# Performance work log

Hardware: AMD Instinct MI355X
Metric: run time of the kernel (lower is better)

The kernel has to match this reference:

```python
import jax, jax.numpy as jnp
import numpy as np

N, E, ESM, H, OUT, L, NG = 20000, 640000, 1280, 128, 256, 3, 64
NV, EV = 4, 1  # node/edge vector channels
MSG_S, MSG_V = 2 * H + H, 2 * NV + EV   # 384, 9
UPD_S, UPD_V = 2 * H, 2 * NV            # 256, 8


def _safe_norm(v):
    # exact ||v|| with zero (not nan) gradient at v == 0
    n2 = jnp.sum(v * v, axis=-1)
    pos = n2 > 0
    return jnp.sqrt(jnp.where(pos, n2, 1.0)) * pos


def _normalize(x, eps=1e-12):
    n = _safe_norm(x)[..., None]
    return jnp.where(n > 0, x / jnp.maximum(n, eps), 0.0)


def _ln(x, g, b, eps=1e-5):
    m = x.mean(-1, keepdims=True)
    v = ((x - m) ** 2).mean(-1, keepdims=True)
    return (x - m) / jnp.sqrt(v + eps) * g + b


def _gvp(s, v, Wss, Wvs, Wsv, Wvv, g, b):
    # s: [M, Cs], v: [M, Cv, 3]
    vn = _safe_norm(v)                                        # [M, Cv]
    s_out = jax.nn.gelu(_ln(s @ Wss.T + vn @ Wvs.T, g, b), approximate=False)
    v_out = jnp.einsum('mic,oi->moc', v, Wvv)                 # [M, Cvo, 3]
    v_out = v_out * jax.nn.sigmoid(s @ Wsv.T)[:, :, None]     # gate from input s
    return s_out, v_out


def _compute_node_vectors(coords, cb):
    ca_cb = _normalize(cb - coords)
    ca_next = jnp.roll(coords, -1, axis=0)
    d = (ca_next - coords).at[-1].set(0.0)
    d = _normalize(d)
    normal = _normalize(jnp.cross(ca_cb, d))
    t = (ca_next - jnp.roll(coords, 1, axis=0)).at[0].set(0.0).at[-1].set(0.0)
    t = _normalize(t)
    return jnp.stack([ca_cb, d, normal, t], axis=1)           # [N, 4, 3]


def setup_inputs() -> dict:
    key = jax.random.key(0)
    ks = jax.random.split(key, 32)

    def w(k, shape):
        return (jax.random.normal(k, shape, jnp.float32) / np.sqrt(shape[-1])).astype(jnp.float32)

    inp = {
        'esm_features': jax.random.normal(ks[0], (N, ESM), jnp.float32),
        'geometric_features': jax.random.normal(ks[1], (N, 15), jnp.float32),
        'node_coords': jax.random.normal(ks[2], (N, 3), jnp.float32) * 10.0,
        'edge_index': jax.random.randint(ks[3], (2, E), 0, N, jnp.int32),
        'edge_attr': jax.random.normal(ks[4], (E, 16), jnp.float32),
        'batch_index': jnp.sort(jax.random.randint(ks[5], (N,), 0, NG, jnp.int32)),
        # projections
        'node_proj_W': w(ks[6], (H, ESM + 9)), 'node_proj_b': jnp.zeros((H,), jnp.float32),
        'edge_proj_W': w(ks[7], (H, 13)), 'edge_proj_b': jnp.zeros((H,), jnp.float32),
        # message GVP (stacked over L layers)
        'msg_Wss': w(ks[8], (L, H, MSG_S)), 'msg_Wvs': w(ks[9], (L, H, MSG_V)),
        'msg_Wsv': w(ks[10], (L, NV, MSG_S)), 'msg_Wvv': w(ks[11], (L, NV, MSG_V)),
        'msg_ln_g': jnp.ones((L, H), jnp.float32), 'msg_ln_b': jnp.zeros((L, H), jnp.float32),
        # update GVP
        'upd_Wss': w(ks[12], (L, H, UPD_S)), 'upd_Wvs': w(ks[13], (L, H, UPD_V)),
        'upd_Wsv': w(ks[14], (L, NV, UPD_S)), 'upd_Wvv': w(ks[15], (L, NV, UPD_V)),
        'upd_ln_g': jnp.ones((L, H), jnp.float32), 'upd_ln_b': jnp.zeros((L, H), jnp.float32),
        # heads
        'node_out_W': w(ks[16], (ESM, H)), 'node_out_b': jnp.zeros((ESM,), jnp.float32),
        'graph_out_W': w(ks[17], (OUT, H)), 'graph_out_b': jnp.zeros((OUT,), jnp.float32),
    }
    return inp


def reference(esm_features, geometric_features, node_coords, edge_index, edge_attr,
              batch_index, node_proj_W, node_proj_b, edge_proj_W, edge_proj_b,
              msg_Wss, msg_Wvs, msg_Wsv, msg_Wvv, msg_ln_g, msg_ln_b,
              upd_Wss, upd_Wvs, upd_Wsv, upd_Wvv, upd_ln_g, upd_ln_b,
              node_out_W, node_out_b, graph_out_W, graph_out_b):
    n = esm_features.shape[0]
    cb = geometric_features[:, 3:6]
    geo_scalar = geometric_features[:, 6:15]
    node_s = jnp.concatenate([esm_features, geo_scalar], -1) @ node_proj_W.T + node_proj_b
    node_v = _compute_node_vectors(node_coords, cb)
    edge_s = jnp.concatenate([edge_attr[:, 0:2], edge_attr[:, 5:]], -1) @ edge_proj_W.T + edge_proj_b
    edge_v = edge_attr[:, 2:5][:, None, :]                    # [E, 1, 3]
    src, dst = edge_index[0], edge_index[1]
    for l in range(msg_Wss.shape[0]):
        ms = jnp.concatenate([node_s[src], node_s[dst], edge_s], -1)   # [E, 3H]
        mv = jnp.concatenate([node_v[src], node_v[dst], edge_v], 1)    # [E, 9, 3]
        ms, mv = _gvp(ms, mv, msg_Wss[l], msg_Wvs[l], msg_Wsv[l], msg_Wvv[l],
                      msg_ln_g[l], msg_ln_b[l])
        ag_s = jnp.zeros((n, ms.shape[1]), ms.dtype).at[dst].add(ms)
        ag_v = jnp.zeros((n, mv.shape[1], 3), mv.dtype).at[dst].add(mv)
        us = jnp.concatenate([node_s, ag_s], -1)
        uv = jnp.concatenate([node_v, ag_v], 1)
        ns, nv = _gvp(us, uv, upd_Wss[l], upd_Wvs[l], upd_Wsv[l], upd_Wvv[l],
                      upd_ln_g[l], upd_ln_b[l])
        node_s = node_s + ns
        node_v = node_v + nv
    updated_nodes = node_s @ node_out_W.T + node_out_b
    gfeat = node_s @ graph_out_W.T + graph_out_b
    cnt = jax.ops.segment_sum(jnp.ones((n,), gfeat.dtype), batch_index, NG)
    graph_emb = jax.ops.segment_sum(gfeat, batch_index, NG) / jnp.maximum(cnt, 1.0)[:, None]
    return graph_emb, updated_nodes
```

## Files before the change

kernel.cpp:

```cpp
#include <hip/hip_runtime.h>
#include <math.h>

#define DEVI __device__ __forceinline__

namespace {

constexpr int NN = 20000;
constexpr int NE = 640000;

DEVI float gelu_f(float x){ return 0.5f*x*(1.0f+erff(x*0.70710678118654752440f)); }
DEVI float gelu_t(float x){
  float u = x*x;
  float z = x*(1.59576912f + 0.07135481f*u);
  return x / (1.f + __expf(-z));
}
DEVI float sigm(float x){ return 1.0f/(1.0f+expf(-x)); }
DEVI float sigm_f(float x){ return 1.0f/(1.0f+__expf(-x)); }

struct F3{ float x,y,z; };
DEVI F3 sub3(F3 a, F3 b){ return F3{a.x-b.x, a.y-b.y, a.z-b.z}; }
DEVI F3 cross3(F3 a, F3 b){ return F3{a.y*b.z-a.z*b.y, a.z*b.x-a.x*b.z, a.x*b.y-a.y*b.x}; }
DEVI F3 snorm3(F3 v){
  float n2 = v.x*v.x+v.y*v.y+v.z*v.z;
  if(n2 > 0.f){ float inv = 1.0f/sqrtf(n2); return F3{v.x*inv, v.y*inv, v.z*inv}; }
  return F3{0.f,0.f,0.f};
}

__global__ void k_prep(const float* __restrict__ npW, const float* __restrict__ noW,
                       const float* __restrict__ goW,
                       const float* __restrict__ mWss, const float* __restrict__ mWvs,
                       const float* __restrict__ uWss, const float* __restrict__ uWvs,
                       float* __restrict__ Wt_np, float* __restrict__ Wt_no,
                       float* __restrict__ Wt_go,
                       float* __restrict__ Wt_mss, float* __restrict__ Wt_mvs,
                       float* __restrict__ Wt_uss, float* __restrict__ Wt_uvs){
  int b = blockIdx.x, t = threadIdx.x;
  const float* src; float* dst; int R,C,ld,base,elems;
  if(b<645){ src=npW; dst=Wt_np; R=128;C=1289;ld=1289; base=0; elems=164992; }
  else if(b<1285){ src=noW; dst=Wt_no; R=1280;C=128;ld=128; base=645; elems=163840; }
  else if(b<1413){ src=goW; dst=Wt_go; R=256;C=128;ld=128; base=1285; elems=32768; }
  else {
    int bb=b-1413; int l=bb/265; int r=bb-l*265;
    if(r<128){ src=mWss+(size_t)l*128*384; dst=Wt_mss+(size_t)l*256*128; R=128;C=256;ld=384; base=1413+l*265; elems=32768; }
    else if(r<133){ src=mWvs+(size_t)l*128*9; dst=Wt_mvs+(size_t)l*9*128; R=128;C=9;ld=9; base=1413+l*265+128; elems=1152; }
    else if(r<261){ src=uWss+(size_t)l*128*256; dst=Wt_uss+(size_t)l*256*128; R=128;C=256;ld=256; base=1413+l*265+133; elems=32768; }
    else { src=uWvs+(size_t)l*128*8; dst=Wt_uvs+(size_t)l*8*128; R=128;C=8;ld=8; base=1413+l*265+261; elems=1024; }
  }
  int idx=(b-base)*256+t;
  if(idx>=elems) return;
  int r=idx/C, c=idx%C;
  dst[c*R+r] = src[r*ld+c];
}

__global__ __launch_bounds__(256,4) void k_init(
                       const float* __restrict__ esm, const float* __restrict__ geo,
                       const float* __restrict__ Wt, const float* __restrict__ bias,
                       float* __restrict__ node_s){
  __shared__ float s_l[16][64];
  int t = threadIdx.x;
  int o = t&127, h = t>>7;
  int n0 = blockIdx.x*16;
  float acc[8];
#pragma unroll
  for(int i=0;i<8;i++) acc[i]=0.f;
  for(int k0=0;k0<1289;k0+=64){
    int kmax = (1289-k0 < 64) ? (1289-k0) : 64;
    for(int idx=t; idx<1024; idx+=256){
      int n = idx>>6, k = idx&63;
      float v = 0.f;
      int kk = k0+k;
      if(k < kmax){
        v = (kk<1280) ? esm[(size_t)(n0+n)*1280 + kk] : geo[(n0+n)*15 + 6 + (kk-1280)];
      }
      s_l[n][k] = v;
    }
    __syncthreads();
    int kq = kmax & ~3;
    for(int k=0;k<kq;k+=4){
      float w0 = Wt[(k0+k)*128+o];
      float w1 = Wt[(k0+k+1)*128+o];
      float w2 = Wt[(k0+k+2)*128+o];
      float w3 = Wt[(k0+k+3)*128+o];
#pragma unroll
      for(int n=0;n<8;n++){
        float4 s4 = *reinterpret_cast<const float4*>(&s_l[h*8+n][k]);
        acc[n] += s4.x*w0 + s4.y*w1 + s4.z*w2 + s4.w*w3;
      }
    }
    for(int k=kq;k<kmax;k++){
      float w = Wt[(k0+k)*128+o];
#pragma unroll
      for(int n=0;n<8;n++) acc[n] += s_l[h*8+n][k]*w;
    }
    __syncthreads();
  }
  float b = bias[o];
#pragma unroll
  for(int n=0;n<8;n++) node_s[(size_t)(n0+h*8+n)*128 + o] = acc[n] + b;
}

__global__ void k_nodevec(const float* __restrict__ coords, const float* __restrict__ geo,
                          float* __restrict__ node_v,
                          int* __restrict__ counts, int* __restrict__ cntg){
  int n = blockIdx.x*256 + threadIdx.x;
  if(n<64) cntg[n]=0;
  if(n>=NN) return;
  counts[n]=0;
  F3 c  {coords[n*3], coords[n*3+1], coords[n*3+2]};
  F3 cb {geo[n*15+3], geo[n*15+4], geo[n*15+5]};
  F3 cacb = snorm3(sub3(cb, c));
  F3 d{0.f,0.f,0.f};
  if(n < NN-1){
    F3 nx {coords[(n+1)*3], coords[(n+1)*3+1], coords[(n+1)*3+2]};
    d = snorm3(sub3(nx, c));
  }
  F3 nor = snorm3(cross3(cacb, d));
  F3 tv{0.f,0.f,0.f};
  if(n>0 && n<NN-1){
    F3 nx {coords[(n+1)*3], coords[(n+1)*3+1], coords[(n+1)*3+2]};
    F3 pv {coords[(n-1)*3], coords[(n-1)*3+1], coords[(n-1)*3+2]};
    tv = snorm3(sub3(nx, pv));
  }
  float* p = node_v + n*12;
  p[0]=cacb.x; p[1]=cacb.y; p[2]=cacb.z;
  p[3]=d.x;    p[4]=d.y;    p[5]=d.z;
  p[6]=nor.x;  p[7]=nor.y;  p[8]=nor.z;
  p[9]=tv.x;   p[10]=tv.y;  p[11]=tv.z;
}

__global__ void k_hist(const int* __restrict__ eidx, const int* __restrict__ batch,
                       int* __restrict__ counts, int* __restrict__ cntg){
  int i = blockIdx.x*256+threadIdx.x;
  if(i<NE) atomicAdd(&counts[eidx[NE+i]], 1);
  if(i<NN) atomicAdd(&cntg[batch[i]], 1);
}
__global__ void k_scan1(const int* __restrict__ counts, int* __restrict__ bsums){
  __shared__ int red[256];
  int b=blockIdx.x, t=threadIdx.x;
  int base=b*512;
  int v=0;
  for(int i=t;i<512;i+=256){ int g=base+i; if(g<NN) v+=counts[g]; }
  red[t]=v; __syncthreads();
  for(int s=128;s;s>>=1){ if(t<s) red[t]+=red[t+s]; __syncthreads(); }
  if(t==0) bsums[b]=red[0];
}
__global__ void k_scan23(const int* __restrict__ counts, const int* __restrict__ bsums,
                         int* __restrict__ offs, int* __restrict__ cursor){
  __shared__ int c_l[512];
  int b=blockIdx.x, t=threadIdx.x, base=b*512;
  for(int i=t;i<512;i+=256){ int g=base+i; c_l[i] = (g<NN)? counts[g]:0; }
  __syncthreads();
  if(t==0){
    int run=0;
    for(int i=0;i<b;i++) run += bsums[i];
    for(int i=0;i<512;i++){
      int g=base+i;
      if(g<NN){ offs[g]=run; cursor[g]=run; }
      run += c_l[i];
    }
    if(b==39) offs[NN]=run;
  }
}
__global__ void k_fill(const int* __restrict__ eidx, int* __restrict__ cursor,
                       const float* __restrict__ eattr,
                       int* __restrict__ srcp, float* __restrict__ ea_s){
  int e = blockIdx.x*256+threadIdx.x;
  if(e>=NE) return;
  int d = eidx[NE+e];
  int s = eidx[e];
  int pos = atomicAdd(&cursor[d], 1);
  srcp[pos] = s;
  const float4* src4 = reinterpret_cast<const float4*>(eattr + (size_t)e*16);
  float4* dst4 = reinterpret_cast<float4*>(ea_s + (size_t)pos*16);
  dst4[0]=src4[0]; dst4[1]=src4[1]; dst4[2]=src4[2]; dst4[3]=src4[3];
}

__global__ __launch_bounds__(256,4) void k_pre(
                      const float* __restrict__ node_s, const float* __restrict__ node_v,
                      const float* __restrict__ Wt_ss, const float* __restrict__ Wt_vs,
                      const float* __restrict__ Wsv, const float* __restrict__ Wvv,
                      float* __restrict__ P_a, float* __restrict__ P_b,
                      float* __restrict__ G_a, float* __restrict__ G_b,
                      float* __restrict__ V_a, float* __restrict__ V_b){
  __shared__ float s_l[16][128];
  __shared__ float nv_l[16][4];
  __shared__ float uv[16][12];
  int t = threadIdx.x;
  int n0 = blockIdx.x*16;
  for(int idx=t; idx<2048; idx+=256){
    int n = idx>>7, k = idx&127;
    s_l[n][k] = node_s[(size_t)(n0+n)*128 + k];
  }
  if(t<192){ int n=t/12, k=t%12; uv[n][k] = node_v[(n0+n)*12+k]; }
  __syncthreads();
  if(t<64){
    int n=t>>2, j=t&3;
    float x=uv[n][j*3], y=uv[n][j*3+1], z=uv[n][j*3+2];
    float n2=x*x+y*y+z*z;
    nv_l[n][j] = n2>0.f ? sqrtf(n2) : 0.f;
  }
  if(t<192){
    int n=t/12, k=t%12, c=k/3, x=k-c*3;
    float va=0.f, vb=0.f;
#pragma unroll
    for(int j=0;j<4;j++){
      float vv = uv[n][j*3+x];
      va += Wvv[c*9+j]*vv;
      vb += Wvv[c*9+4+j]*vv;
    }
    V_a[(n0+n)*12+k]=va; V_b[(n0+n)*12+k]=vb;
  }
  if(t<128){
    int n=t>>3, c=(t>>1)&3, hh=t&1;
    const float* w = Wsv + c*384 + hh*128;
    float g=0.f;
    for(int k=0;k<128;k++) g += s_l[n][k]*w[k];
    (hh ? G_b : G_a)[(n0+n)*4+c] = g;
  }
  __syncthreads();
  int o = t&127, h = t>>7;
  float acc[16];
#pragma unroll
  for(int i=0;i<16;i++) acc[i]=0.f;
  const float* Wb = Wt_ss + h*128*128;
  for(int k=0;k<128;k++){
    float w = Wb[k*128+o];
#pragma unroll
    for(int n=0;n<16;n++) acc[n] += s_l[n][k]*w;
  }
  const float* Wv = Wt_vs + h*4*128;
#pragma unroll
  for(int j=0;j<4;j++){
    float w = Wv[j*128+o];
#pragma unroll
    for(int n=0;n<16;n++) acc[n] += nv_l[n][j]*w;
  }
  float* P = h ? P_b : P_a;
#pragma unroll
  for(int n=0;n<16;n++) P[(size_t)(n0+n)*128+o] = acc[n];
}

__global__ void k_econst3(const float* __restrict__ mWss, const float* __restrict__ mWvs,
                          const float* __restrict__ mWsv, const float* __restrict__ mWvv,
                          const float* __restrict__ Wep, const float* __restrict__ epb,
                          float* __restrict__ econ){
  int l = blockIdx.x;
  const float* Wss = mWss + (size_t)l*128*384;
  const float* Wvs = mWvs + (size_t)l*128*9;
  const float* Wsv = mWsv + (size_t)l*4*384;
  const float* Wvv = mWvv + (size_t)l*4*9;
  float* ec = econ + (size_t)l*2048;
  int t=threadIdx.x;
  for(int idx=t; idx<13*128; idx+=256){
    int j=idx>>7, o=idx&127;
    float s=0.f;
    for(int k=0;k<128;k++) s += Wss[o*384+256+k]*Wep[k*13+j];
    ec[j*128+o]=s;
  }
  for(int o=t;o<128;o+=256){
    float s=0.f;
    for(int k=0;k<128;k++) s += Wss[o*384+256+k]*epb[k];
    ec[1664+o]=s;
    ec[1792+o]=Wvs[o*9+8];
  }
  if(t<52){ int c=t/13,j=t%13; float s=0.f; for(int k=0;k<128;k++) s+=Wsv[c*384+256+k]*Wep[k*13+j]; ec[1920+t]=s; }
  if(t<4){ float s=0.f; for(int k=0;k<128;k++) s+=Wsv[t*384+256+k]*epb[k]; ec[1972+t]=s; ec[1976+t]=Wvv[t*9+8]; }
}

#define DECLST(P) int P##s=0; float4 P##A0{},P##A1{},P##A2{},P##A3{}; \
                  float P##pax=0.f,P##pay=0.f,P##ga=0.f,P##va=0.f;
#define LOADST(P, IDX) do{ int _p=(IDX); \
  P##s = srcp[_p]; \
  const float4* _ea = reinterpret_cast<const float4*>(ea_s + (size_t)_p*16); \
  P##A0=_ea[0]; P##A1=_ea[1]; P##A2=_ea[2]; P##A3=_ea[3]; \
  const float* _pa = P_a + (size_t)P##s*128; \
  P##pax=_pa[lane]; P##pay=_pa[64+lane]; \
  if(lane<12){ P##ga=G_a[(size_t)P##s*4+cv]; P##va=V_a[(size_t)P##s*12+lane]; } \
}while(0)
#define COMPUTE(P) do{ \
  float e0=P##A0.x,e1=P##A0.y,e2=P##A1.y,e3=P##A1.z,e4=P##A1.w, \
        e5=P##A2.x,e6=P##A2.y,e7=P##A2.z,e8=P##A2.w,e9=P##A3.x, \
        e10=P##A3.y,e11=P##A3.z,e12=P##A3.w; \
  float evx=P##A0.z, evy=P##A0.w, evz=P##A1.x; \
  float en2 = evx*evx+evy*evy+evz*evz; \
  float evn = en2>0.f ? sqrtf(en2) : 0.f; \
  float px = fmaf(evn,W8x, P##pax + Bx); \
  float py = fmaf(evn,W8y, P##pay + By); \
  px=fmaf(me2x[0],e0,px);   py=fmaf(me2y[0],e0,py); \
  px=fmaf(me2x[1],e1,px);   py=fmaf(me2y[1],e1,py); \
  px=fmaf(me2x[2],e2,px);   py=fmaf(me2y[2],e2,py); \
  px=fmaf(me2x[3],e3,px);   py=fmaf(me2y[3],e3,py); \
  px=fmaf(me2x[4],e4,px);   py=fmaf(me2y[4],e4,py); \
  px=fmaf(me2x[5],e5,px);   py=fmaf(me2y[5],e5,py); \
  px=fmaf(me2x[6],e6,px);   py=fmaf(me2y[6],e6,py); \
  px=fmaf(me2x[7],e7,px);   py=fmaf(me2y[7],e7,py); \
  px=fmaf(me2x[8],e8,px);   py=fmaf(me2y[8],e8,py); \
  px=fmaf(me2x[9],e9,px);   py=fmaf(me2y[9],e9,py); \
  px=fmaf(me2x[10],e10,px); py=fmaf(me2y[10],e10,py); \
  px=fmaf(me2x[11],e11,px); py=fmaf(me2y[11],e11,py); \
  px=fmaf(me2x[12],e12,px); py=fmaf(me2y[12],e12,py); \
  float sm = px+py; \
  float sq = px*px + py*py; \
  _Pragma("unroll") \
  for(int m=32;m;m>>=1){ sm += __shfl_xor(sm,m); sq += __shfl_xor(sq,m); } \
  float mean = sm*0.0078125f; \
  float var  = fmaf(sq,0.0078125f, -mean*mean); \
  float rstd = rsqrtf((var>0.f?var:0.f) + 1e-5f); \
  accx += gelu_t(fmaf((px-mean)*rstd, LGx, LBx)); \
  accy += gelu_t(fmaf((py-mean)*rstd, LGy, LBy)); \
  if(lane<12){ \
    float g = P##ga + gbc; \
    g=fmaf(grc[0],e0,g); g=fmaf(grc[1],e1,g); g=fmaf(grc[2],e2,g); \
    g=fmaf(grc[3],e3,g); g=fmaf(grc[4],e4,g); g=fmaf(grc[5],e5,g); \
    g=fmaf(grc[6],e6,g); g=fmaf(grc[7],e7,g); g=fmaf(grc[8],e8,g); \
    g=fmaf(grc[9],e9,g); g=fmaf(grc[10],e10,g); g=fmaf(grc[11],e11,g); \
    g=fmaf(grc[12],e12,g); \
    float gt = sigm_f(g); \
    float evc = (xv==0) ? evx : ((xv==1) ? evy : evz); \
    avk = fmaf(fmaf(wvc,evc, P##va + vbk), gt, avk); \
  } \
}while(0)

__global__ __launch_bounds__(256,2) void k_msg(
                      const float* __restrict__ P_a, const float* __restrict__ P_b,
                      const float* __restrict__ G_a, const float* __restrict__ G_b,
                      const float* __restrict__ V_a, const float* __restrict__ V_b,
                      const float* __restrict__ ea_s, const int* __restrict__ srcp,
                      const int* __restrict__ offs,
                      const float* __restrict__ ec,
                      const float* __restrict__ lng, const float* __restrict__ lnb,
                      float* __restrict__ ag_s, float* __restrict__ ag_v){
  int t = threadIdx.x;
  int n = blockIdx.x*4 + (t>>6);
  int lane = t&63;
  float me2x[13], me2y[13];
#pragma unroll
  for(int j=0;j<13;j++){ me2x[j]=ec[j*128+lane]; me2y[j]=ec[j*128+64+lane]; }
  float Bx = ec[1664+lane]    + P_b[(size_t)n*128+lane];
  float By = ec[1664+64+lane] + P_b[(size_t)n*128+64+lane];
  float W8x = ec[1792+lane], W8y = ec[1792+64+lane];
  float LGx = lng[lane], LGy = lng[64+lane];
  float LBx = lnb[lane], LBy = lnb[64+lane];
  int cv = lane/3, xv = lane - cv*3;
  int cvg = (lane<12) ? cv : 0;
  float grc[13];
#pragma unroll
  for(int j=0;j<13;j++) grc[j] = ec[1920 + cvg*13 + j];
  float vbk=0.f, gbc=0.f, wvc=0.f;
  if(lane<12){
    vbk = V_b[(size_t)n*12+lane];
    gbc = G_b[(size_t)n*4+cv] + ec[1972+cv];
    wvc = ec[1976+cv];
  }
  float accx=0.f, accy=0.f, avk=0.f;
  int beg = offs[n], end = offs[n+1];
  DECLST(a_) DECLST(b_)
  int idx = beg;
  if(beg < end) LOADST(a_, beg);
  while(idx + 1 < end){
    LOADST(b_, idx+1);
    COMPUTE(a_);
    if(idx + 2 < end) LOADST(a_, idx+2);
    COMPUTE(b_);
    idx += 2;
  }
  if(idx < end) COMPUTE(a_);
  ag_s[(size_t)n*128+lane]    = accx;
  ag_s[(size_t)n*128+64+lane] = accy;
  if(lane<12) ag_v[(size_t)n*12+lane] = avk;
}

__global__ __launch_bounds__(256,4) void k_update(
                         float* __restrict__ node_s, float* __restrict__ node_v,
                         const float* __restrict__ ag_s, const float* __restrict__ ag_v,
                         const float* __restrict__ Wt_ss, const float* __restrict__ Wt_vs,
                         const float* __restrict__ Wsv, const float* __restrict__ Wvv,
                         const float* __restrict__ lng, const float* __restrict__ lnb){
  __shared__ float us[16][257];
  __shared__ float pre[16][129];
  __shared__ float uv[16][24];
  __shared__ float uvn[16][8];
  __shared__ float stats[16][2];
  __shared__ float gate_l[16][4];
  int t = threadIdx.x;
  int n0 = blockIdx.x*16;
  for(int idx=t; idx<2048; idx+=256){
    int n = idx>>7, k = idx&127;
    us[n][k]     = node_s[(size_t)(n0+n)*128+k];
    us[n][128+k] = ag_s[(size_t)(n0+n)*128+k];
  }
  for(int idx=t; idx<384; idx+=256){
    int n = idx/24, k = idx%24;
    uv[n][k] = (k<12) ? node_v[(n0+n)*12+k] : ag_v[(n0+n)*12 + (k-12)];
  }
  __syncthreads();
  if(t<128){
    int n=t>>3, j=t&7;
    float x=uv[n][j*3], y=uv[n][j*3+1], z=uv[n][j*3+2];
    float n2=x*x+y*y+z*z;
    uvn[n][j] = n2>0.f ? sqrtf(n2) : 0.f;
  }
  __syncthreads();
  int o = t&127, h = t>>7;
  float acc[8];
#pragma unroll
  for(int i=0;i<8;i++) acc[i]=0.f;
  for(int k=0;k<256;k++){
    float w = Wt_ss[k*128+o];
#pragma unroll
    for(int i=0;i<8;i++) acc[i] += us[h*8+i][k]*w;
  }
#pragma unroll
  for(int j=0;j<8;j++){
    float w = Wt_vs[j*128+o];
#pragma unroll
    for(int i=0;i<8;i++) acc[i] += uvn[h*8+i][j]*w;
  }
#pragma unroll
  for(int i=0;i<8;i++) pre[h*8+i][o] = acc[i];
  __syncthreads();
  {
    int n = t>>4, p = t&15;
    float s=0.f;
#pragma unroll
    for(int q=0;q<8;q++) s += pre[n][p*8+q];
#pragma unroll
    for(int m=8;m;m>>=1) s += __shfl_xor(s,m);
    float mean = s*(1.f/128.f);
    float v=0.f;
#pragma unroll
    for(int q=0;q<8;q++){ float d=pre[n][p*8+q]-mean; v += d*d; }
#pragma unroll
    for(int m=8;m;m>>=1) v += __shfl_xor(v,m);
    if(p==0){ stats[n][0]=mean; stats[n][1]=rsqrtf(v*(1.f/128.f)+1e-5f); }
  }
  __syncthreads();
  {
    float LG = lng[o], LB = lnb[o];
#pragma unroll
    for(int i=0;i<8;i++){
      int n = h*8+i;
      float hh = (pre[n][o]-stats[n][0])*stats[n][1]*LG + LB;
      node_s[(size_t)(n0+n)*128+o] += gelu_f(hh);
    }
  }
  {
    int n = t>>4, c = t&3, p = (t>>2)&3;
    float g=0.f;
    int kb = p*64;
    for(int k=0;k<64;k++) g += us[n][kb+k]*Wsv[c*256+kb+k];
    g += __shfl_xor(g,4);
    g += __shfl_xor(g,8);
    if(p==0) gate_l[n][c] = sigm(g);
  }
  __syncthreads();
  if(t<192){
    int n = t/12, k = t%12, c = k/3, x = k-c*3;
    float s=0.f;
#pragma unroll
    for(int j=0;j<8;j++) s += Wvv[c*8+j]*uv[n][j*3+x];
    node_v[(n0+n)*12+k] += s*gate_l[n][c];
  }
}

__global__ __launch_bounds__(256,4) void k_outg(
                      const float* __restrict__ node_s, const float* __restrict__ Wt_no,
                      const float* __restrict__ nob, const float* __restrict__ Wt_go,
                      const int* __restrict__ batch, float* __restrict__ gacc,
                      float* __restrict__ out){
  __shared__ float s_l[16][128];
  __shared__ int b_l[16];
  int t = threadIdx.x;
  int n0 = blockIdx.x*16;
  int y = blockIdx.y;
  for(int idx=t; idx<2048; idx+=256){
    int n=idx>>7, k=idx&127;
    s_l[n][k] = node_s[(size_t)(n0+n)*128+k];
  }
  if(y==5 && t<16) b_l[t]=batch[n0+t];
  __syncthreads();
  if(y<5){
    int o = y*256 + t;
    float acc[16];
#pragma unroll
    for(int i=0;i<16;i++) acc[i]=0.f;
    for(int k=0;k<128;k++){
      float w = Wt_no[k*1280+o];
#pragma unroll
      for(int n=0;n<16;n++) acc[n] += s_l[n][k]*w;
    }
    float b = nob[o];
#pragma unroll
    for(int n=0;n<16;n++) out[16384 + (size_t)(n0+n)*1280 + o] = acc[n]+b;
  } else {
    int o=t;
    float acc[16];
#pragma unroll
    for(int i=0;i<16;i++) acc[i]=0.f;
    for(int k=0;k<128;k++){
      float w=Wt_go[k*256+o];
#pragma unroll
      for(int n=0;n<16;n++) acc[n]+=s_l[n][k]*w;
    }
    float run=0.f; int cur=b_l[0];
#pragma unroll
    for(int n=0;n<16;n++){
      int g=b_l[n];
      if(g!=cur){ atomicAdd(&gacc[cur*256+o], run); run=0.f; cur=g; }
      run += acc[n];
    }
    atomicAdd(&gacc[cur*256+o], run);
  }
}

__global__ void k_gfin(const float* __restrict__ gacc, const int* __restrict__ cntg,
                       const float* __restrict__ gob, float* __restrict__ out){
  int g=blockIdx.x, o=threadIdx.x;
  int c=cntg[g];
  out[g*256+o] = (c>0) ? (gacc[g*256+o]/(float)c + gob[o]) : 0.f;
}

}

extern "C" void kernel_launch(void* const* d_in, const int* in_sizes, int n_in,
                              void* d_out, int out_size, void* d_ws, size_t ws_size,
                              hipStream_t stream){
  (void)in_sizes; (void)n_in; (void)out_size;
  const float* esm   = (const float*)d_in[0];
  const float* geo   = (const float*)d_in[1];
  const float* coords= (const float*)d_in[2];
  const int*   eidx  = (const int*)d_in[3];
  const float* eattr = (const float*)d_in[4];
  const int*   batch = (const int*)d_in[5];
  const float* npW   = (const float*)d_in[6];
  const float* npb   = (const float*)d_in[7];
  const float* epW   = (const float*)d_in[8];
  const float* epb   = (const float*)d_in[9];
  const float* mWss  = (const float*)d_in[10];
  const float* mWvs  = (const float*)d_in[11];
  const float* mWsv  = (const float*)d_in[12];
  const float* mWvv  = (const float*)d_in[13];
  const float* mlg   = (const float*)d_in[14];
  const float* mlb   = (const float*)d_in[15];
  const float* uWss  = (const float*)d_in[16];
  const float* uWvs  = (const float*)d_in[17];
  const float* uWsv  = (const float*)d_in[18];
  const float* uWvv  = (const float*)d_in[19];
  const float* ulg   = (const float*)d_in[20];
  const float* ulb   = (const float*)d_in[21];
  const float* noW   = (const float*)d_in[22];
  const float* nob   = (const float*)d_in[23];
  const float* goW   = (const float*)d_in[24];
  const float* gob   = (const float*)d_in[25];
  float* out = (float*)d_out;

  char* base = (char*)d_ws;
  size_t off = 0;
  auto ALLOC = [&](size_t bytes)->char*{
    char* p = base + off;
    off = (off + bytes + 255) & ~(size_t)255;
    return p;
  };
  float* node_s = (float*)ALLOC((size_t)NN*128*4);
  float* P_a    = (float*)ALLOC((size_t)NN*128*4);
  float* P_b    = (float*)ALLOC((size_t)NN*128*4);
  float* ag_s   = (float*)ALLOC((size_t)NN*128*4);
  float* node_v = (float*)ALLOC((size_t)NN*12*4);
  float* ag_v   = (float*)ALLOC((size_t)NN*12*4);
  float* V_a    = (float*)ALLOC((size_t)NN*12*4);
  float* V_b    = (float*)ALLOC((size_t)NN*12*4);
  float* G_a    = (float*)ALLOC((size_t)NN*4*4);
  float* G_b    = (float*)ALLOC((size_t)NN*4*4);
  float* Wt_np  = (float*)ALLOC((size_t)1289*128*4);
  float* Wt_no  = (float*)ALLOC((size_t)128*1280*4);
  float* Wt_go  = (float*)ALLOC((size_t)128*256*4);
  float* Wt_mss = (float*)ALLOC((size_t)3*256*128*4);
  float* Wt_mvs = (float*)ALLOC((size_t)3*9*128*4);
  float* Wt_uss = (float*)ALLOC((size_t)3*256*128*4);
  float* Wt_uvs = (float*)ALLOC((size_t)3*8*128*4);
  float* econ   = (float*)ALLOC((size_t)3*2048*4);
  float* gacc   = (float*)ALLOC((size_t)64*256*4);
  int* counts = (int*)ALLOC((size_t)NN*4);
  int* offs   = (int*)ALLOC((size_t)(NN+1)*4);
  int* cursor = (int*)ALLOC((size_t)NN*4);
  int* bsums  = (int*)ALLOC((size_t)64*4);
  int* cntg   = (int*)ALLOC((size_t)64*4);
  int* srcp   = (int*)ALLOC((size_t)NE*4);
  float* ea_s = (float*)ALLOC((size_t)NE*16*4);
  if(off > ws_size) return;

  hipMemsetAsync(gacc, 0, (size_t)64*256*4, stream);

  k_prep<<<2208,256,0,stream>>>(npW, noW, goW, mWss, mWvs, uWss, uWvs,
                                Wt_np, Wt_no, Wt_go, Wt_mss, Wt_mvs, Wt_uss, Wt_uvs);
  k_init<<<1250,256,0,stream>>>(esm, geo, Wt_np, npb, node_s);
  k_nodevec<<<79,256,0,stream>>>(coords, geo, node_v, counts, cntg);
  k_hist<<<2500,256,0,stream>>>(eidx, batch, counts, cntg);
  k_scan1<<<40,256,0,stream>>>(counts, bsums);
  k_scan23<<<40,256,0,stream>>>(counts, bsums, offs, cursor);
  k_fill<<<2500,256,0,stream>>>(eidx, cursor, eattr, srcp, ea_s);
  k_econst3<<<3,256,0,stream>>>(mWss, mWvs, mWsv, mWvv, epW, epb, econ);

  for(int l=0;l<3;l++){
    k_pre<<<1250,256,0,stream>>>(node_s, node_v,
                                 Wt_mss + (size_t)l*256*128, Wt_mvs + (size_t)l*9*128,
                                 mWsv + (size_t)l*4*384, mWvv + (size_t)l*4*9,
                                 P_a, P_b, G_a, G_b, V_a, V_b);
    k_msg<<<5000,256,0,stream>>>(P_a, P_b, G_a, G_b, V_a, V_b, ea_s, srcp, offs,
                                 econ + (size_t)l*2048, mlg + (size_t)l*128, mlb + (size_t)l*128,
                                 ag_s, ag_v);
    k_update<<<1250,256,0,stream>>>(node_s, node_v, ag_s, ag_v,
                                    Wt_uss + (size_t)l*256*128, Wt_uvs + (size_t)l*8*128,
                                    uWsv + (size_t)l*4*256, uWvv + (size_t)l*4*8,
                                    ulg + (size_t)l*128, ulb + (size_t)l*128);
  }
  k_outg<<<dim3(1250,6),256,0,stream>>>(node_s, Wt_no, nob, Wt_go, batch, gacc, out);
  k_gfin<<<64,256,0,stream>>>(gacc, cntg, gob, out);
}
```

Before: 1.741 ms.

## Split edge-attribute projection into separate bf16-packed precompute kernel before message pass

Adds a k_edge kernel that computes the per-edge scalar projection (edge attributes times the folded message weights) and the gate/vector edge terms, storing the scalar part as packed bf16 pairs. k_msg then reads these precomputed values instead of recomputing 13-term FMAs per lane, frees registers and raises launch bounds occupancy to 4. In exchange it writes and reads roughly 164MB of extra traffic per layer and adds bf16 rounding error to the pre-LayerNorm activations. Several small GEMV inner loops are also changed to read shared-memory rows as float4 and the shared array is padded for alignment.

```diff
diff --git a/kernel.cpp b/kernel.cpp
--- a/kernel.cpp
+++ b/kernel.cpp
@@ -16,6 +16,7 @@
 }
 DEVI float sigm(float x){ return 1.0f/(1.0f+expf(-x)); }
 DEVI float sigm_f(float x){ return 1.0f/(1.0f+__expf(-x)); }
+DEVI unsigned bf_rne(float f){ unsigned u=__float_as_uint(f); return (u + 0x7fffu + ((u>>16)&1u)) >> 16; }
 
 struct F3{ float x,y,z; };
 DEVI F3 sub3(F3 a, F3 b){ return F3{a.x-b.x, a.y-b.y, a.z-b.z}; }
@@ -214,7 +215,11 @@
     int n=t>>3, c=(t>>1)&3, hh=t&1;
     const float* w = Wsv + c*384 + hh*128;
     float g=0.f;
-    for(int k=0;k<128;k++) g += s_l[n][k]*w[k];
+    for(int k=0;k<128;k+=4){
+      float4 s4 = *reinterpret_cast<const float4*>(&s_l[n][k]);
+      g = fmaf(s4.x,w[k],g); g = fmaf(s4.y,w[k+1],g);
+      g = fmaf(s4.z,w[k+2],g); g = fmaf(s4.w,w[k+3],g);
+    }
     (hh ? G_b : G_a)[(n0+n)*4+c] = g;
   }
   __syncthreads();
@@ -223,10 +228,14 @@
 #pragma unroll
   for(int i=0;i<16;i++) acc[i]=0.f;
   const float* Wb = Wt_ss + h*128*128;
-  for(int k=0;k<128;k++){
-    float w = Wb[k*128+o];
-#pragma unroll
-    for(int n=0;n<16;n++) acc[n] += s_l[n][k]*w;
+  for(int k=0;k<128;k+=4){
+    float w0=Wb[(k+0)*128+o], w1=Wb[(k+1)*128+o], w2=Wb[(k+2)*128+o], w3=Wb[(k+3)*128+o];
+#pragma unroll
+    for(int n=0;n<16;n++){
+      float4 s4 = *reinterpret_cast<const float4*>(&s_l[n][k]);
+      acc[n] = fmaf(s4.x,w0,acc[n]); acc[n] = fmaf(s4.y,w1,acc[n]);
+      acc[n] = fmaf(s4.z,w2,acc[n]); acc[n] = fmaf(s4.w,w3,acc[n]);
+    }
   }
   const float* Wv = Wt_vs + h*4*128;
 #pragma unroll
@@ -267,89 +276,113 @@
   if(t<4){ float s=0.f; for(int k=0;k<128;k++) s+=Wsv[t*384+256+k]*epb[k]; ec[1972+t]=s; ec[1976+t]=Wvv[t*9+8]; }
 }
 
-#define DECLST(P) int P##s=0; float4 P##A0{},P##A1{},P##A2{},P##A3{}; \
-                  float P##pax=0.f,P##pay=0.f,P##ga=0.f,P##va=0.f;
-#define LOADST(P, IDX) do{ int _p=(IDX); \
-  P##s = srcp[_p]; \
-  const float4* _ea = reinterpret_cast<const float4*>(ea_s + (size_t)_p*16); \
-  P##A0=_ea[0]; P##A1=_ea[1]; P##A2=_ea[2]; P##A3=_ea[3]; \
-  const float* _pa = P_a + (size_t)P##s*128; \
-  P##pax=_pa[lane]; P##pay=_pa[64+lane]; \
-  if(lane<12){ P##ga=G_a[(size_t)P##s*4+cv]; P##va=V_a[(size_t)P##s*12+lane]; } \
+__global__ __launch_bounds__(256,4) void k_edge(
+    const float* __restrict__ ea_s, const float* __restrict__ ec,
+    unsigned* __restrict__ preS2, float* __restrict__ preG){
+  int t = threadIdx.x;
+  int lane = t&63;
+  int wid = blockIdx.x*4 + (t>>6);
+  float mex[13], mey[13];
+#pragma unroll
+  for(int j=0;j<13;j++){ mex[j]=ec[j*128+lane]; mey[j]=ec[j*128+64+lane]; }
+  float bx=ec[1664+lane], by=ec[1664+64+lane];
+  float w8x=ec[1792+lane], w8y=ec[1792+64+lane];
+  int cg = (lane<4)?lane:0;
+  float grc[13];
+#pragma unroll
+  for(int j=0;j<13;j++) grc[j]=ec[1920+cg*13+j];
+  float gb = ec[1972+cg];
+  int e00 = wid*8;
+#pragma unroll 2
+  for(int i=0;i<8;i++){
+    int e = e00+i;
+    const float4* ea = reinterpret_cast<const float4*>(ea_s + (size_t)e*16);
+    float4 A0=ea[0], A1=ea[1], A2=ea[2], A3=ea[3];
+    float e0=A0.x,e1=A0.y,e2=A1.y,e3=A1.z,e4=A1.w,
+          e5=A2.x,e6=A2.y,e7=A2.z,e8=A2.w,e9=A3.x,
+          e10=A3.y,e11=A3.z,e12=A3.w;
+    float evx=A0.z, evy=A0.w, evz=A1.x;
+    float en2 = evx*evx+evy*evy+evz*evz;
+    float evn = en2>0.f ? sqrtf(en2) : 0.f;
+    float px = fmaf(evn,w8x,bx);
+    float py = fmaf(evn,w8y,by);
+    px=fmaf(mex[0],e0,px);   py=fmaf(mey[0],e0,py);
+    px=fmaf(mex[1],e1,px);   py=fmaf(mey[1],e1,py);
+    px=fmaf(mex[2],e2,px);   py=fmaf(mey[2],e2,py);
+    px=fmaf(mex[3],e3,px);   py=fmaf(mey[3],e3,py);
+    px=fmaf(mex[4],e4,px);   py=fmaf(mey[4],e4,py);
+    px=fmaf(mex[5],e5,px);   py=fmaf(mey[5],e5,py);
+    px=fmaf(mex[6],e6,px);   py=fmaf(mey[6],e6,py);
+    px=fmaf(mex[7],e7,px);   py=fmaf(mey[7],e7,py);
+    px=fmaf(mex[8],e8,px);   py=fmaf(mey[8],e8,py);
+    px=fmaf(mex[9],e9,px);   py=fmaf(mey[9],e9,py);
+    px=fmaf(mex[10],e10,px); py=fmaf(mey[10],e10,py);
+    px=fmaf(mex[11],e11,px); py=fmaf(mey[11],e11,py);
+    px=fmaf(mex[12],e12,px); py=fmaf(mey[12],e12,py);
+    preS2[(size_t)e*64+lane] = bf_rne(px) | (bf_rne(py)<<16);
+    if(lane<4){
+      float g=gb;
+      g=fmaf(grc[0],e0,g);  g=fmaf(grc[1],e1,g);  g=fmaf(grc[2],e2,g);
+      g=fmaf(grc[3],e3,g);  g=fmaf(grc[4],e4,g);  g=fmaf(grc[5],e5,g);
+      g=fmaf(grc[6],e6,g);  g=fmaf(grc[7],e7,g);  g=fmaf(grc[8],e8,g);
+      g=fmaf(grc[9],e9,g);  g=fmaf(grc[10],e10,g); g=fmaf(grc[11],e11,g);
+      g=fmaf(grc[12],e12,g);
+      preG[(size_t)e*8+lane] = g;
+    } else if(lane<7){
+      float evv = (lane==4)?evx:((lane==5)?evy:evz);
+      preG[(size_t)e*8+lane] = evv;
+    }
+  }
+}
+
+#define DECLST(P) unsigned P##w=0; float P##pax=0.f,P##pay=0.f,P##g8=0.f,P##ev=0.f,P##ga=0.f,P##va=0.f;
+#define LOADST(P, IDX) do{ int _p=(IDX); int _s=srcp[_p]; \
+  P##w   = preS2[(size_t)_p*64 + lane]; \
+  P##pax = P_a[(size_t)_s*128+lane]; P##pay = P_a[(size_t)_s*128+64+lane]; \
+  if(lane<12){ P##g8 = preG[(size_t)_p*8+cv]; P##ev = preG[(size_t)_p*8+4+xv]; \
+               P##ga = G_a[(size_t)_s*4+cv];  P##va = V_a[(size_t)_s*12+lane]; } \
 }while(0)
 #define COMPUTE(P) do{ \
-  float e0=P##A0.x,e1=P##A0.y,e2=P##A1.y,e3=P##A1.z,e4=P##A1.w, \
-        e5=P##A2.x,e6=P##A2.y,e7=P##A2.z,e8=P##A2.w,e9=P##A3.x, \
-        e10=P##A3.y,e11=P##A3.z,e12=P##A3.w; \
-  float evx=P##A0.z, evy=P##A0.w, evz=P##A1.x; \
-  float en2 = evx*evx+evy*evy+evz*evz; \
-  float evn = en2>0.f ? sqrtf(en2) : 0.f; \
-  float px = fmaf(evn,W8x, P##pax + Bx); \
-  float py = fmaf(evn,W8y, P##pay + By); \
-  px=fmaf(me2x[0],e0,px);   py=fmaf(me2y[0],e0,py); \
-  px=fmaf(me2x[1],e1,px);   py=fmaf(me2y[1],e1,py); \
-  px=fmaf(me2x[2],e2,px);   py=fmaf(me2y[2],e2,py); \
-  px=fmaf(me2x[3],e3,px);   py=fmaf(me2y[3],e3,py); \
-  px=fmaf(me2x[4],e4,px);   py=fmaf(me2y[4],e4,py); \
-  px=fmaf(me2x[5],e5,px);   py=fmaf(me2y[5],e5,py); \
-  px=fmaf(me2x[6],e6,px);   py=fmaf(me2y[6],e6,py); \
-  px=fmaf(me2x[7],e7,px);   py=fmaf(me2y[7],e7,py); \
-  px=fmaf(me2x[8],e8,px);   py=fmaf(me2y[8],e8,py); \
-  px=fmaf(me2x[9],e9,px);   py=fmaf(me2y[9],e9,py); \
-  px=fmaf(me2x[10],e10,px); py=fmaf(me2y[10],e10,py); \
-  px=fmaf(me2x[11],e11,px); py=fmaf(me2y[11],e11,py); \
-  px=fmaf(me2x[12],e12,px); py=fmaf(me2y[12],e12,py); \
-  float sm = px+py; \
-  float sq = px*px + py*py; \
+  float px = __uint_as_float(P##w<<16); \
+  float py = __uint_as_float(P##w & 0xffff0000u); \
+  float pre0 = px + P##pax + PBx; \
+  float pre1 = py + P##pay + PBy; \
+  float sm = pre0+pre1; \
+  float sq = pre0*pre0 + pre1*pre1; \
   _Pragma("unroll") \
   for(int m=32;m;m>>=1){ sm += __shfl_xor(sm,m); sq += __shfl_xor(sq,m); } \
   float mean = sm*0.0078125f; \
   float var  = fmaf(sq,0.0078125f, -mean*mean); \
   float rstd = rsqrtf((var>0.f?var:0.f) + 1e-5f); \
-  accx += gelu_t(fmaf((px-mean)*rstd, LGx, LBx)); \
-  accy += gelu_t(fmaf((py-mean)*rstd, LGy, LBy)); \
+  accx += gelu_t(fmaf((pre0-mean)*rstd, LGx, LBx)); \
+  accy += gelu_t(fmaf((pre1-mean)*rstd, LGy, LBy)); \
   if(lane<12){ \
-    float g = P##ga + gbc; \
-    g=fmaf(grc[0],e0,g); g=fmaf(grc[1],e1,g); g=fmaf(grc[2],e2,g); \
-    g=fmaf(grc[3],e3,g); g=fmaf(grc[4],e4,g); g=fmaf(grc[5],e5,g); \
-    g=fmaf(grc[6],e6,g); g=fmaf(grc[7],e7,g); g=fmaf(grc[8],e8,g); \
-    g=fmaf(grc[9],e9,g); g=fmaf(grc[10],e10,g); g=fmaf(grc[11],e11,g); \
-    g=fmaf(grc[12],e12,g); \
+    float g = P##g8 + P##ga + gbn; \
     float gt = sigm_f(g); \
-    float evc = (xv==0) ? evx : ((xv==1) ? evy : evz); \
-    avk = fmaf(fmaf(wvc,evc, P##va + vbk), gt, avk); \
+    avk = fmaf(fmaf(wvc, P##ev, P##va + vbk), gt, avk); \
   } \
 }while(0)
 
-__global__ __launch_bounds__(256,2) void k_msg(
+__global__ __launch_bounds__(256,4) void k_msg(
                       const float* __restrict__ P_a, const float* __restrict__ P_b,
                       const float* __restrict__ G_a, const float* __restrict__ G_b,
                       const float* __restrict__ V_a, const float* __restrict__ V_b,
-                      const float* __restrict__ ea_s, const int* __restrict__ srcp,
-                      const int* __restrict__ offs,
+                      const unsigned* __restrict__ preS2, const float* __restrict__ preG,
+                      const int* __restrict__ srcp, const int* __restrict__ offs,
                       const float* __restrict__ ec,
                       const float* __restrict__ lng, const float* __restrict__ lnb,
                       float* __restrict__ ag_s, float* __restrict__ ag_v){
   int t = threadIdx.x;
   int n = blockIdx.x*4 + (t>>6);
   int lane = t&63;
-  float me2x[13], me2y[13];
-#pragma unroll
-  for(int j=0;j<13;j++){ me2x[j]=ec[j*128+lane]; me2y[j]=ec[j*128+64+lane]; }
-  float Bx = ec[1664+lane]    + P_b[(size_t)n*128+lane];
-  float By = ec[1664+64+lane] + P_b[(size_t)n*128+64+lane];
-  float W8x = ec[1792+lane], W8y = ec[1792+64+lane];
+  float PBx = P_b[(size_t)n*128+lane], PBy = P_b[(size_t)n*128+64+lane];
   float LGx = lng[lane], LGy = lng[64+lane];
   float LBx = lnb[lane], LBy = lnb[64+lane];
   int cv = lane/3, xv = lane - cv*3;
-  int cvg = (lane<12) ? cv : 0;
-  float grc[13];
-#pragma unroll
-  for(int j=0;j<13;j++) grc[j] = ec[1920 + cvg*13 + j];
-  float vbk=0.f, gbc=0.f, wvc=0.f;
+  float vbk=0.f, gbn=0.f, wvc=0.f;
   if(lane<12){
     vbk = V_b[(size_t)n*12+lane];
-    gbc = G_b[(size_t)n*4+cv] + ec[1972+cv];
+    gbn = G_b[(size_t)n*4+cv];
     wvc = ec[1976+cv];
   }
   float accx=0.f, accy=0.f, avk=0.f;
@@ -376,7 +409,7 @@
                          const float* __restrict__ Wt_ss, const float* __restrict__ Wt_vs,
                          const float* __restrict__ Wsv, const float* __restrict__ Wvv,
                          const float* __restrict__ lng, const float* __restrict__ lnb){
-  __shared__ float us[16][257];
+  __shared__ float us[16][260];
   __shared__ float pre[16][129];
   __shared__ float uv[16][24];
   __shared__ float uvn[16][8];
@@ -405,10 +438,14 @@
   float acc[8];
 #pragma unroll
   for(int i=0;i<8;i++) acc[i]=0.f;
-  for(int k=0;k<256;k++){
-    float w = Wt_ss[k*128+o];
-#pragma unroll
-    for(int i=0;i<8;i++) acc[i] += us[h*8+i][k]*w;
+  for(int k=0;k<256;k+=4){
+    float w0=Wt_ss[(k+0)*128+o], w1=Wt_ss[(k+1)*128+o], w2=Wt_ss[(k+2)*128+o], w3=Wt_ss[(k+3)*128+o];
+#pragma unroll
+    for(int i=0;i<8;i++){
+      float4 s4 = *reinterpret_cast<const float4*>(&us[h*8+i][k]);
+      acc[i] = fmaf(s4.x,w0,acc[i]); acc[i] = fmaf(s4.y,w1,acc[i]);
+      acc[i] = fmaf(s4.z,w2,acc[i]); acc[i] = fmaf(s4.w,w3,acc[i]);
+    }
   }
 #pragma unroll
   for(int j=0;j<8;j++){
@@ -448,7 +485,11 @@
     int n = t>>4, c = t&3, p = (t>>2)&3;
     float g=0.f;
     int kb = p*64;
-    for(int k=0;k<64;k++) g += us[n][kb+k]*Wsv[c*256+kb+k];
+    for(int k=0;k<64;k+=4){
+      float4 s4 = *reinterpret_cast<const float4*>(&us[n][kb+k]);
+      g = fmaf(s4.x,Wsv[c*256+kb+k],g);   g = fmaf(s4.y,Wsv[c*256+kb+k+1],g);
+      g = fmaf(s4.z,Wsv[c*256+kb+k+2],g); g = fmaf(s4.w,Wsv[c*256+kb+k+3],g);
+    }
     g += __shfl_xor(g,4);
     g += __shfl_xor(g,8);
     if(p==0) gate_l[n][c] = sigm(g);
@@ -484,10 +525,14 @@
     float acc[16];
 #pragma unroll
     for(int i=0;i<16;i++) acc[i]=0.f;
-    for(int k=0;k<128;k++){
-      float w = Wt_no[k*1280+o];
-#pragma unroll
-      for(int n=0;n<16;n++) acc[n] += s_l[n][k]*w;
+    for(int k=0;k<128;k+=4){
+      float w0=Wt_no[(k+0)*1280+o], w1=Wt_no[(k+1)*1280+o], w2=Wt_no[(k+2)*1280+o], w3=Wt_no[(k+3)*1280+o];
+#pragma unroll
+      for(int n=0;n<16;n++){
+        float4 s4 = *reinterpret_cast<const float4*>(&s_l[n][k]);
+        acc[n] = fmaf(s4.x,w0,acc[n]); acc[n] = fmaf(s4.y,w1,acc[n]);
+        acc[n] = fmaf(s4.z,w2,acc[n]); acc[n] = fmaf(s4.w,w3,acc[n]);
+      }
     }
     float b = nob[o];
 #pragma unroll
@@ -497,10 +542,14 @@
     float acc[16];
 #pragma unroll
     for(int i=0;i<16;i++) acc[i]=0.f;
-    for(int k=0;k<128;k++){
-      float w=Wt_go[k*256+o];
-#pragma unroll
-      for(int n=0;n<16;n++) acc[n]+=s_l[n][k]*w;
+    for(int k=0;k<128;k+=4){
+      float w0=Wt_go[(k+0)*256+o], w1=Wt_go[(k+1)*256+o], w2=Wt_go[(k+2)*256+o], w3=Wt_go[(k+3)*256+o];
+#pragma unroll
+      for(int n=0;n<16;n++){
+        float4 s4 = *reinterpret_cast<const float4*>(&s_l[n][k]);
+        acc[n] = fmaf(s4.x,w0,acc[n]); acc[n] = fmaf(s4.y,w1,acc[n]);
+        acc[n] = fmaf(s4.z,w2,acc[n]); acc[n] = fmaf(s4.w,w3,acc[n]);
+      }
     }
     float run=0.f; int cur=b_l[0];
 #pragma unroll
@@ -587,6 +636,8 @@
   int* cntg   = (int*)ALLOC((size_t)64*4);
   int* srcp   = (int*)ALLOC((size_t)NE*4);
   float* ea_s = (float*)ALLOC((size_t)NE*16*4);
+  unsigned* preS2 = (unsigned*)ALLOC((size_t)NE*64*4);
+  float* preG     = (float*)ALLOC((size_t)NE*8*4);
   if(off > ws_size) return;
 
   hipMemsetAsync(gacc, 0, (size_t)64*256*4, stream);
@@ -606,7 +657,8 @@
                                  Wt_mss + (size_t)l*256*128, Wt_mvs + (size_t)l*9*128,
                                  mWsv + (size_t)l*4*384, mWvv + (size_t)l*4*9,
                                  P_a, P_b, G_a, G_b, V_a, V_b);
-    k_msg<<<5000,256,0,stream>>>(P_a, P_b, G_a, G_b, V_a, V_b, ea_s, srcp, offs,
+    k_edge<<<20000,256,0,stream>>>(ea_s, econ + (size_t)l*2048, preS2, preG);
+    k_msg<<<5000,256,0,stream>>>(P_a, P_b, G_a, G_b, V_a, V_b, preS2, preG, srcp, offs,
                                  econ + (size_t)l*2048, mlg + (size_t)l*128, mlb + (size_t)l*128,
                                  ag_s, ag_v);
     k_update<<<1250,256,0,stream>>>(node_s, node_v, ag_s, ag_v,
```

New measurement: 1.716 ms. Within noise of the previous version (-1.4%).
